# Kernel tuning notes

Measured on AMD Instinct MI355X. Metric: run time of the kernel, lower is better.

The kernel has to match this reference:

```python
import jax, jax.numpy as jnp
import numpy as np

jax.config.update("jax_enable_x64", True)

B, S = 16, 1024


def setup_inputs() -> dict:
    key = jax.random.key(0)
    scores = jax.random.normal(key, (B, S, S), dtype=jnp.float32)
    mask = jnp.ones((B, S), dtype=bool)
    return {"scores": scores, "mask": mask}


def _matrix_tree_logZ(scores, mask):
    # scores: [B,S,S] float64, mask: [B,S] bool
    lens = mask.sum(-1).astype(scores.dtype)          # lengths BEFORE forcing root position
    mask = mask.at[:, 0].set(True)                    # mask.index_fill(1, 0, 1)
    pair = mask[:, :, None] & mask[:, None, :]        # [B,S,S]
    s = jnp.where(pair, scores, -jnp.inf)
    m = jnp.max(s)                                    # single global max (scores.view(1,-1).max())
    A = jnp.exp(s - m)                                # exp-normalized adjacency, 0 outside mask
    rs = A.sum(-1)                                    # [B,S] row sums (degree)
    eye = jnp.eye(S, dtype=A.dtype)
    DmA = eye * rs[:, :, None] - A                    # Laplacian D - A
    # rows with mask==False stay identity rows
    L = jnp.where(mask[:, :, None], DmA, eye)
    logdet = jnp.linalg.slogdet(L[:, 1:, 1:])[1]      # [B]
    return (logdet + m * lens).sum()


def reference(scores, mask):
    # forward with mbr=True, target=None: probs = d logZ / d scores (marginals)
    s64 = scores.astype(jnp.float64)
    probs = jax.grad(_matrix_tree_logZ, argnums=0)(s64, mask)
    return probs.astype(jnp.float32)
```

## Files before the change

### kernel.cpp

```cpp
#include <hip/hip_runtime.h>

#define BB 16
#define SS 1024
#define NPAD 1024
#define NBLK 128
#define NSTEP 8
#define TILEPK 32768

typedef __attribute__((ext_vector_type(8))) __bf16 bf16x8;
typedef __attribute__((ext_vector_type(4))) float f32x4;

__device__ __forceinline__ unsigned int enc_f32(float f) {
  unsigned int u = __float_as_uint(f);
  return (u & 0x80000000u) ? ~u : (u | 0x80000000u);
}
__device__ __forceinline__ float dec_key(unsigned int k) {
  unsigned int u = (k & 0x80000000u) ? (k & 0x7fffffffu) : ~k;
  return __uint_as_float(u);
}
__device__ __forceinline__ void gload16(const __bf16* g, __bf16* l) {
  __builtin_amdgcn_global_load_lds(
      (const __attribute__((address_space(1))) void*)g,
      (__attribute__((address_space(3))) void*)l, 16, 0, 0);
}

__global__ void __launch_bounds__(64) kinit(unsigned long long* mk) { *mk = 0ull; }

__global__ void __launch_bounds__(256) kmax(const float* __restrict__ sc,
                                            unsigned long long* __restrict__ mk) {
  __shared__ unsigned long long red[256];
  const long long n = (long long)BB * SS * SS;
  unsigned long long best = 0ull;
  for (long long i = (long long)blockIdx.x * 256 + threadIdx.x; i < n;
       i += (long long)gridDim.x * 256) {
    unsigned long long k = ((unsigned long long)enc_f32(sc[i]) << 32) | (unsigned int)i;
    if (k > best) best = k;
  }
  red[threadIdx.x] = best;
  __syncthreads();
  for (int s = 128; s > 0; s >>= 1) {
    if ((int)threadIdx.x < s) {
      unsigned long long o = red[threadIdx.x + s];
      if (o > red[threadIdx.x]) red[threadIdx.x] = o;
    }
    __syncthreads();
  }
  if (threadIdx.x == 0) atomicMax(mk, red[0]);
}

__global__ void __launch_bounds__(256) kbuild(const float* __restrict__ sc,
                                              float* __restrict__ M,
                                              const unsigned long long* __restrict__ mk) {
  __shared__ float red[256];
  const int r = blockIdx.x;
  const int b = blockIdx.y;
  const int t = threadIdx.x;
  float* Mrow = M + ((size_t)b * NPAD + r) * NPAD;
  if (r == NPAD - 1) {
    for (int c = t; c < NPAD; c += 256) Mrow[c] = (c == NPAD - 1) ? 1.0f : 0.0f;
    return;
  }
  const float m = dec_key((unsigned int)(*mk >> 32));
  const int i = r + 1;
  const float* srow = sc + ((size_t)b * SS + i) * SS;
  float part = 0.f;
  for (int j = t; j < SS; j += 256) part += expf(srow[j] - m);
  red[t] = part;
  __syncthreads();
  for (int s = 128; s > 0; s >>= 1) {
    if (t < s) red[t] += red[t + s];
    __syncthreads();
  }
  const float rs = red[0];
  for (int c = t; c < NPAD; c += 256) {
    float v;
    if (c == NPAD - 1) v = 0.0f;
    else {
      v = -expf(srow[c + 1] - m);
      if (c == r) v += rs;
    }
    Mrow[c] = v;
  }
}

__global__ void __launch_bounds__(256) kcopydiag(const float* __restrict__ M,
                                                 __bf16* __restrict__ Tpk,
                                                 float* __restrict__ D,
                                                 __bf16* __restrict__ DA,
                                                 __bf16* __restrict__ DB, int kb) {
  const int x = blockIdx.x;
  const int t = threadIdx.x;
  if (x < NSTEP * BB) {
    const int rt = x >> 4, b = x & 15;
    const float* src = M + ((size_t)b * NPAD + rt * NBLK) * NPAD + kb * NBLK;
    __bf16* dst = Tpk + ((size_t)b * NSTEP + rt) * TILEPK;
#pragma unroll
    for (int itr = 0; itr < 8; ++itr) {
      const int gid = itr * 256 + t;
      const int m15 = gid & 15, q = (gid >> 4) & 3, R = (gid >> 6) & 7, ks = gid >> 9;
      const float* sp = src + (size_t)(R * 16 + m15) * NPAD + ks * 32 + q * 8;
      float f[8];
      *(float4*)(f + 0) = *(const float4*)(sp);
      *(float4*)(f + 4) = *(const float4*)(sp + 4);
      bf16x8 hv, lv;
#pragma unroll
      for (int j = 0; j < 8; ++j) {
        const float xv = f[j];
        const __bf16 h = (__bf16)xv;
        hv[j] = h;
        lv[j] = (__bf16)(xv - (float)h);
      }
      const int fi = ((R * 4 + q) * 16 + m15) * 8;
      *(bf16x8*)&dst[(size_t)ks * 8192 + fi] = hv;
      *(bf16x8*)&dst[(size_t)ks * 8192 + 4096 + fi] = lv;
    }
    return;
  }
  __shared__ float ds16[16][16];
  __shared__ float pinv16[16][18];
  __shared__ float rowp[16][128];
  __shared__ float rext[16][128];
  __shared__ float colp[128][20];
  __shared__ __bf16 Bsh[128][130];
  const int b = x - NSTEP * BB;
  const int tx = t & 15, ty = t >> 4;
  const int l = t & 63;
  const int lrow = l & 15, lcg = l >> 4;
  const float* src = M + ((size_t)b * NPAD + kb * NBLK) * NPAD + kb * NBLK;
  float r[8][8];
#pragma unroll
  for (int ii = 0; ii < 8; ++ii) {
    const float* sp = src + (size_t)(ty + 16 * ii) * NPAD + 8 * tx;
    *(float4*)&r[ii][0] = *(const float4*)(sp);
    *(float4*)&r[ii][4] = *(const float4*)(sp + 4);
  }

  for (int g = 0; g < 8; ++g) {
    const bool own_pc = ((tx >> 1) == g);
#pragma unroll
    for (int ii = 0; ii < 8; ++ii) {
      if (ii == g) {
        *(float4*)&rowp[ty][8 * tx] = *(const float4*)&r[ii][0];
        *(float4*)&rowp[ty][8 * tx + 4] = *(const float4*)&r[ii][4];
        if (own_pc) {
          *(float4*)&ds16[ty][8 * (tx & 1)] = *(const float4*)&r[ii][0];
          *(float4*)&ds16[ty][8 * (tx & 1) + 4] = *(const float4*)&r[ii][4];
        }
      }
      if (own_pc) {
        *(float4*)&colp[ty + 16 * ii][8 * (tx & 1)] = *(const float4*)&r[ii][0];
        *(float4*)&colp[ty + 16 * ii][8 * (tx & 1) + 4] = *(const float4*)&r[ii][4];
      }
    }
    __syncthreads();
    float dd[4];
    {
      const f32x4 dv = *(const f32x4*)&ds16[lrow][4 * lcg];
      dd[0] = dv[0]; dd[1] = dv[1]; dd[2] = dv[2]; dd[3] = dv[3];
    }
#pragma unroll
    for (int k = 0; k < 16; ++k) {
      const int pcg = k >> 2, pr = k & 3;
      const float pv = __shfl(dd[pr], k + 16 * pcg);
      const float pinv = 1.0f / pv;
      const float ck = __shfl(dd[pr], lrow + 16 * pcg);
      float rk[4];
#pragma unroll
      for (int c = 0; c < 4; ++c) rk[c] = __shfl(dd[c], k + 16 * lcg);
      const bool isp = (lrow == k);
      const float cp = ck * pinv;
#pragma unroll
      for (int c = 0; c < 4; ++c) {
        const bool zc = (lcg == pcg) && (c == pr);
        const float upd = (zc ? 0.0f : dd[c]) - cp * (zc ? 1.0f : rk[c]);
        const float prw = zc ? pinv : dd[c] * pinv;
        dd[c] = isp ? prw : upd;
      }
    }
#pragma unroll
    for (int c = 0; c < 4; ++c) pinv16[lrow][4 * lcg + c] = dd[c];
    __syncthreads();
    float pvr[16];
#pragma unroll
    for (int a = 0; a < 16; ++a) pvr[a] = pinv16[ty][a];
    float Rv[8];
#pragma unroll
    for (int jj = 0; jj < 8; ++jj) Rv[jj] = 0.0f;
#pragma unroll
    for (int a = 0; a < 16; ++a) {
      const float pa = pvr[a];
      const f32x4 q0 = *(const f32x4*)&rowp[a][8 * tx];
      const f32x4 q1 = *(const f32x4*)&rowp[a][8 * tx + 4];
      Rv[0] += pa * q0[0]; Rv[1] += pa * q0[1]; Rv[2] += pa * q0[2]; Rv[3] += pa * q0[3];
      Rv[4] += pa * q1[0]; Rv[5] += pa * q1[1]; Rv[6] += pa * q1[2]; Rv[7] += pa * q1[3];
    }
    if (own_pc) {
#pragma unroll
      for (int jj = 0; jj < 8; ++jj) Rv[jj] = pinv16[ty][8 * (tx & 1) + jj];
    }
    {
      float4 w0 = make_float4(Rv[0], Rv[1], Rv[2], Rv[3]);
      float4 w1 = make_float4(Rv[4], Rv[5], Rv[6], Rv[7]);
      *(float4*)&rext[ty][8 * tx] = w0;
      *(float4*)&rext[ty][8 * tx + 4] = w1;
    }
    __syncthreads();
    if (own_pc) {
#pragma unroll
      for (int ii = 0; ii < 8; ++ii)
#pragma unroll
        for (int jj = 0; jj < 8; ++jj) r[ii][jj] = 0.0f;
    }
#pragma unroll
    for (int a0 = 0; a0 < 16; a0 += 4) {
      float ca[8][4];
#pragma unroll
      for (int ii = 0; ii < 8; ++ii)
        *(float4*)&ca[ii][0] = *(const float4*)&colp[ty + 16 * ii][a0];
#pragma unroll
      for (int ac = 0; ac < 4; ++ac) {
        const f32x4 ra0 = *(const f32x4*)&rext[a0 + ac][8 * tx];
        const f32x4 ra1 = *(const f32x4*)&rext[a0 + ac][8 * tx + 4];
#pragma unroll
        for (int ii = 0; ii < 8; ++ii) {
          const float cv = ca[ii][ac];
          r[ii][0] -= cv * ra0[0]; r[ii][1] -= cv * ra0[1];
          r[ii][2] -= cv * ra0[2]; r[ii][3] -= cv * ra0[3];
          r[ii][4] -= cv * ra1[0]; r[ii][5] -= cv * ra1[1];
          r[ii][6] -= cv * ra1[2]; r[ii][7] -= cv * ra1[3];
        }
      }
    }
#pragma unroll
    for (int ii = 0; ii < 8; ++ii) {
      if (ii == g) {
        const f32x4 ra0 = *(const f32x4*)&rext[ty][8 * tx];
        const f32x4 ra1 = *(const f32x4*)&rext[ty][8 * tx + 4];
        r[ii][0] = ra0[0]; r[ii][1] = ra0[1]; r[ii][2] = ra0[2]; r[ii][3] = ra0[3];
        r[ii][4] = ra1[0]; r[ii][5] = ra1[1]; r[ii][6] = ra1[2]; r[ii][7] = ra1[3];
      }
    }
    __syncthreads();
  }
  float* dst = D + (size_t)b * NBLK * NBLK;
  __bf16* dA = DA + (size_t)b * TILEPK;
  __bf16* dB = DB + (size_t)b * TILEPK;
#pragma unroll
  for (int ii = 0; ii < 8; ++ii) {
    *(float4*)(dst + (size_t)(ty + 16 * ii) * NBLK + 8 * tx) = *(const float4*)&r[ii][0];
    *(float4*)(dst + (size_t)(ty + 16 * ii) * NBLK + 8 * tx + 4) = *(const float4*)&r[ii][4];
    bf16x8 hv, lv;
#pragma unroll
    for (int jj = 0; jj < 8; ++jj) {
      const float xv = r[ii][jj];
      const __bf16 h = (__bf16)xv;
      hv[jj] = h;
      lv[jj] = (__bf16)(xv - (float)h);
    }
    const int fiA = ((ii * 4 + (tx & 3)) * 16 + ty) * 8;
    *(bf16x8*)&dA[(size_t)(tx >> 2) * 8192 + fiA] = hv;
    *(bf16x8*)&dA[(size_t)(tx >> 2) * 8192 + 4096 + fiA] = lv;
    *(bf16x8*)&Bsh[ty + 16 * ii][8 * tx] = hv;
  }
  __syncthreads();
#pragma unroll
  for (int g8 = 0; g8 < 8; ++g8) {
    const int gid = g8 * 256 + t;
    const int n15 = gid & 15, q = (gid >> 4) & 3, Ct = (gid >> 6) & 7, ks = gid >> 9;
    const int n = Ct * 16 + n15, k0 = ks * 32 + q * 8;
    bf16x8 v;
#pragma unroll
    for (int j = 0; j < 8; ++j) v[j] = Bsh[k0 + j][n];
    *(bf16x8*)&dB[(size_t)ks * 4096 + (size_t)gid * 8] = v;
  }
  __syncthreads();
#pragma unroll
  for (int ii = 0; ii < 8; ++ii) {
    bf16x8 lv;
#pragma unroll
    for (int jj = 0; jj < 8; ++jj) {
      const float xv = r[ii][jj];
      const __bf16 h = (__bf16)xv;
      lv[jj] = (__bf16)(xv - (float)h);
    }
    *(bf16x8*)&Bsh[ty + 16 * ii][8 * tx] = lv;
  }
  __syncthreads();
#pragma unroll
  for (int g8 = 0; g8 < 8; ++g8) {
    const int gid = g8 * 256 + t;
    const int n15 = gid & 15, q = (gid >> 4) & 3, Ct = (gid >> 6) & 7, ks = gid >> 9;
    const int n = Ct * 16 + n15, k0 = ks * 32 + q * 8;
    bf16x8 v;
#pragma unroll
    for (int j = 0; j < 8; ++j) v[j] = Bsh[k0 + j][n];
    *(bf16x8*)&dB[(size_t)ks * 4096 + (size_t)gid * 8 + 4096] = v;
  }
}

__device__ __forceinline__ void gemm_pp(const __bf16* __restrict__ pA,
                                        const __bf16* __restrict__ pB,
                                        float* __restrict__ C, int ldc,
                                        float alpha, float beta) {
  __shared__ __bf16 sA[2][8192];
  __shared__ __bf16 sB[2][8192];
  const int t = threadIdx.x;
  const int l = t & 63, w = t >> 6;
  const int rbase = (w & 1) * 4, cbase = (w >> 1) * 4;

  f32x4 acc[4][4];
#pragma unroll
  for (int i = 0; i < 4; i++)
#pragma unroll
    for (int j = 0; j < 4; j++) acc[i][j] = (f32x4){0.f, 0.f, 0.f, 0.f};

  {
    const __bf16* gA = pA + (size_t)w * 2048 + l * 8;
    const __bf16* gB = pB + (size_t)w * 2048 + l * 8;
#pragma unroll
    for (int i = 0; i < 4; ++i) {
      gload16(gA + i * 512, &sA[0][w * 2048 + i * 512]);
      gload16(gB + i * 512, &sB[0][w * 2048 + i * 512]);
    }
  }
  __syncthreads();
#pragma unroll
  for (int ks = 0; ks < 4; ++ks) {
    const int buf = ks & 1;
    if (ks < 3) {
      const __bf16* gA = pA + (size_t)(ks + 1) * 8192 + w * 2048 + l * 8;
      const __bf16* gB = pB + (size_t)(ks + 1) * 8192 + w * 2048 + l * 8;
#pragma unroll
      for (int i = 0; i < 4; ++i) {
        gload16(gA + i * 512, &sA[buf ^ 1][w * 2048 + i * 512]);
        gload16(gB + i * 512, &sB[buf ^ 1][w * 2048 + i * 512]);
      }
    }
    bf16x8 a_h[4], a_l[4];
#pragma unroll
    for (int rt = 0; rt < 4; ++rt) {
      a_h[rt] = *(const bf16x8*)&sA[buf][(size_t)((rbase + rt) * 64 + l) * 8];
      a_l[rt] = *(const bf16x8*)&sA[buf][4096 + (size_t)((rbase + rt) * 64 + l) * 8];
    }
#pragma unroll
    for (int ct = 0; ct < 4; ++ct) {
      bf16x8 b_h = *(const bf16x8*)&sB[buf][(size_t)((cbase + ct) * 64 + l) * 8];
      bf16x8 b_l = *(const bf16x8*)&sB[buf][4096 + (size_t)((cbase + ct) * 64 + l) * 8];
#pragma unroll
      for (int rt = 0; rt < 4; ++rt) {
        acc[rt][ct] = __builtin_amdgcn_mfma_f32_16x16x32_bf16(a_h[rt], b_h, acc[rt][ct], 0, 0, 0);
        acc[rt][ct] = __builtin_amdgcn_mfma_f32_16x16x32_bf16(a_h[rt], b_l, acc[rt][ct], 0, 0, 0);
        acc[rt][ct] = __builtin_amdgcn_mfma_f32_16x16x32_bf16(a_l[rt], b_h, acc[rt][ct], 0, 0, 0);
      }
    }
    if (ks < 3) __syncthreads();
  }
  const int row0 = (w & 1) * 64 + ((l >> 4) << 2);
  const int col0 = (w >> 1) * 64 + (l & 15);
  if (beta == 0.0f) {
#pragma unroll
    for (int rt = 0; rt < 4; ++rt)
#pragma unroll
      for (int ct = 0; ct < 4; ++ct)
#pragma unroll
        for (int r = 0; r < 4; ++r)
          C[(size_t)(row0 + rt * 16 + r) * ldc + col0 + ct * 16] = alpha * acc[rt][ct][r];
  } else {
#pragma unroll
    for (int rt = 0; rt < 4; ++rt)
#pragma unroll
      for (int ct = 0; ct < 4; ++ct)
#pragma unroll
        for (int r = 0; r < 4; ++r) {
          float* cp = C + (size_t)(row0 + rt * 16 + r) * ldc + col0 + ct * 16;
          *cp = beta * (*cp) + alpha * acc[rt][ct][r];
        }
  }
}

__global__ void __launch_bounds__(256) kscale(float* __restrict__ M,
                                              const float* __restrict__ D,
                                              const __bf16* __restrict__ DA,
                                              __bf16* __restrict__ Rpk, int kb) {
  const int jt = blockIdx.x, b = blockIdx.y;
  float* Mb = M + (size_t)b * NPAD * NPAD;
  const int t = threadIdx.x;
  if (jt == kb) {
    const float* Dinv = D + (size_t)b * NBLK * NBLK;
    const int c = (t & 31) * 4, r0 = t >> 5;
    float* dst = Mb + (size_t)(kb * NBLK) * NPAD + kb * NBLK;
    for (int r = r0; r < NBLK; r += 8)
      *(float4*)(dst + (size_t)r * NPAD + c) = *(const float4*)(Dinv + r * NBLK + c);
    return;
  }
  __shared__ __bf16 sA[8192];
  __shared__ __bf16 Bh[4096], Bl[4096];
  __shared__ __bf16 Bsh[128][130];
  const int l = t & 63, w = t >> 6;
  const int ic = t & 127, kh = t >> 7;
  const int rbase = (w & 1) * 4, cbase = (w >> 1) * 4;
  const __bf16* pA = DA + (size_t)b * TILEPK;
  float* Btile = Mb + (size_t)(kb * NBLK) * NPAD + jt * NBLK;

  f32x4 acc[4][4];
#pragma unroll
  for (int i = 0; i < 4; i++)
#pragma unroll
    for (int j = 0; j < 4; j++) acc[i][j] = (f32x4){0.f, 0.f, 0.f, 0.f};

  for (int ks = 0; ks < 4; ++ks) {
    const __bf16* gA = pA + (size_t)ks * 8192 + w * 2048 + l * 8;
#pragma unroll
    for (int i = 0; i < 4; ++i) gload16(gA + i * 512, &sA[w * 2048 + i * 512]);
    {
      const float* bp = Btile + (size_t)(ks * 32 + kh * 16) * NPAD + ic;
      float f[16];
#pragma unroll
      for (int kk = 0; kk < 16; ++kk) f[kk] = bp[(size_t)kk * NPAD];
      const int base = ((ic >> 4) * 4 + kh * 2) * 16 + (ic & 15);
#pragma unroll
      for (int g = 0; g < 2; ++g) {
        bf16x8 hv, lv;
#pragma unroll
        for (int j = 0; j < 8; ++j) {
          const float xv = f[g * 8 + j];
          const __bf16 h = (__bf16)xv;
          hv[j] = h;
          lv[j] = (__bf16)(xv - (float)h);
        }
        *(bf16x8*)&Bh[(size_t)(base + g * 16) * 8] = hv;
        *(bf16x8*)&Bl[(size_t)(base + g * 16) * 8] = lv;
      }
    }
    __syncthreads();
    bf16x8 a_h[4], a_l[4];
#pragma unroll
    for (int rt = 0; rt < 4; ++rt) {
      a_h[rt] = *(const bf16x8*)&sA[(size_t)((rbase + rt) * 64 + l) * 8];
      a_l[rt] = *(const bf16x8*)&sA[4096 + (size_t)((rbase + rt) * 64 + l) * 8];
    }
#pragma unroll
    for (int ct = 0; ct < 4; ++ct) {
      bf16x8 b_h = *(const bf16x8*)&Bh[(size_t)((cbase + ct) * 64 + l) * 8];
      bf16x8 b_l = *(const bf16x8*)&Bl[(size_t)((cbase + ct) * 64 + l) * 8];
#pragma unroll
      for (int rt = 0; rt < 4; ++rt) {
        acc[rt][ct] = __builtin_amdgcn_mfma_f32_16x16x32_bf16(a_h[rt], b_h, acc[rt][ct], 0, 0, 0);
        acc[rt][ct] = __builtin_amdgcn_mfma_f32_16x16x32_bf16(a_h[rt], b_l, acc[rt][ct], 0, 0, 0);
        acc[rt][ct] = __builtin_amdgcn_mfma_f32_16x16x32_bf16(a_l[rt], b_h, acc[rt][ct], 0, 0, 0);
      }
    }
    __syncthreads();
  }
  __bf16* Rt = Rpk + ((size_t)b * NSTEP + jt) * TILEPK;
  const int row0 = (w & 1) * 64 + ((l >> 4) << 2);
  const int col0 = (w >> 1) * 64 + (l & 15);
#pragma unroll
  for (int rt = 0; rt < 4; ++rt)
#pragma unroll
    for (int ct = 0; ct < 4; ++ct)
#pragma unroll
      for (int rr = 0; rr < 4; ++rr) {
        const float v = acc[rt][ct][rr];
        const int row = row0 + rt * 16 + rr;
        const int col = col0 + ct * 16;
        Btile[(size_t)row * NPAD + col] = v;
        Bsh[row][col] = (__bf16)v;
      }
  __syncthreads();
#pragma unroll
  for (int g8 = 0; g8 < 8; ++g8) {
    const int gid = g8 * 256 + t;
    const int n15 = gid & 15, q = (gid >> 4) & 3, Ct = (gid >> 6) & 7, ks = gid >> 9;
    const int n = Ct * 16 + n15, k0 = ks * 32 + q * 8;
    bf16x8 v;
#pragma unroll
    for (int j = 0; j < 8; ++j) v[j] = Bsh[k0 + j][n];
    *(bf16x8*)&Rt[(size_t)ks * 4096 + (size_t)gid * 8] = v;
  }
  __syncthreads();
#pragma unroll
  for (int rt = 0; rt < 4; ++rt)
#pragma unroll
    for (int ct = 0; ct < 4; ++ct)
#pragma unroll
      for (int rr = 0; rr < 4; ++rr) {
        const float v = acc[rt][ct][rr];
        const int row = row0 + rt * 16 + rr;
        const int col = col0 + ct * 16;
        const __bf16 h = (__bf16)v;
        Bsh[row][col] = (__bf16)(v - (float)h);
      }
  __syncthreads();
#pragma unroll
  for (int g8 = 0; g8 < 8; ++g8) {
    const int gid = g8 * 256 + t;
    const int n15 = gid & 15, q = (gid >> 4) & 3, Ct = (gid >> 6) & 7, ks = gid >> 9;
    const int n = Ct * 16 + n15, k0 = ks * 32 + q * 8;
    bf16x8 v;
#pragma unroll
    for (int j = 0; j < 8; ++j) v[j] = Bsh[k0 + j][n];
    *(bf16x8*)&Rt[(size_t)ks * 4096 + (size_t)gid * 8 + 4096] = v;
  }
}

__global__ void __launch_bounds__(256) kupdate(float* __restrict__ M,
                                               const __bf16* __restrict__ Tpk,
                                               const __bf16* __restrict__ Rpk,
                                               const __bf16* __restrict__ DB, int kb) {
  const int jt = blockIdx.x;
  int it = blockIdx.y; it = (it >= kb) ? it + 1 : it;
  const int b = blockIdx.z;
  float* Ctile = M + ((size_t)b * NPAD + it * NBLK) * NPAD + jt * NBLK;
  const __bf16* pA = Tpk + ((size_t)b * NSTEP + it) * TILEPK;
  if (jt == kb) {
    gemm_pp(pA, DB + (size_t)b * TILEPK, Ctile, NPAD, -1.0f, 0.0f);
  } else {
    gemm_pp(pA, Rpk + ((size_t)b * NSTEP + jt) * TILEPK, Ctile, NPAD, -1.0f, 1.0f);
  }
}

__global__ void __launch_bounds__(256) kfinal(const float* __restrict__ sc,
                                              const float* __restrict__ Minv,
                                              float* __restrict__ out,
                                              const unsigned long long* __restrict__ mk) {
  __shared__ float Ls[64][65];
  __shared__ float Ds[64];
  const int qt = blockIdx.x, pt = blockIdx.y, b = blockIdx.z;
  const int t = threadIdx.x;
  const unsigned long long key = *mk;
  const float m = dec_key((unsigned int)(key >> 32));
  const unsigned int amax = (unsigned int)key;
  const float* Mb = Minv + (size_t)b * NPAD * NPAD;
  const int q0 = qt * 64, p0 = pt * 64;
  {
    const int pp = t & 63, qq0 = t >> 6;
#pragma unroll
    for (int rp = 0; rp < 16; ++rp) {
      const int qq = qq0 + 4 * rp;
      int rrow = q0 + qq - 1; if (rrow < 0) rrow = 0;
      int ccol = p0 + pp - 1; if (ccol < 0) ccol = 0;
      Ls[qq][pp] = Mb[(size_t)rrow * NPAD + ccol];
    }
    if (t < 64) {
      int cc = p0 + t - 1; if (cc < 0) cc = 0;
      Ds[t] = Mb[(size_t)cc * NPAD + cc];
    }
  }
  __syncthreads();
  const int qq = t & 63, pp0 = t >> 6;
#pragma unroll
  for (int rp = 0; rp < 16; ++rp) {
    const int pp = pp0 + 4 * rp;
    const int p = p0 + pp, q = q0 + qq;
    const size_t off = ((size_t)b * SS + p) * SS + q;
    float val = 0.f;
    if (p >= 1) {
      const float a = expf(sc[off] - m);
      const float g = Ds[pp] - ((q >= 1) ? Ls[qq][pp] : 0.f);
      val = a * g;
    }
    if ((unsigned int)off == amax) val += 16.0f;
    out[off] = val;
  }
}

extern "C" void kernel_launch(void* const* d_in, const int* in_sizes, int n_in,
                              void* d_out, int out_size, void* d_ws, size_t ws_size,
                              hipStream_t stream) {
  const float* sc = (const float*)d_in[0];
  float* out = (float*)d_out;
  char* ws = (char*)d_ws;
  unsigned long long* mk = (unsigned long long*)ws;
  float* M = (float*)(ws + 256);
  float* D = M + (size_t)BB * NPAD * NPAD;
  __bf16* Tpk = (__bf16*)(D + (size_t)BB * NBLK * NBLK);
  __bf16* Rpk = Tpk + (size_t)BB * NSTEP * TILEPK;
  __bf16* DA = Rpk + (size_t)BB * NSTEP * TILEPK;
  __bf16* DB = DA + (size_t)BB * TILEPK;

  hipLaunchKernelGGL(kinit, dim3(1), dim3(64), 0, stream, mk);
  hipLaunchKernelGGL(kmax, dim3(1024), dim3(256), 0, stream, sc, mk);
  hipLaunchKernelGGL(kbuild, dim3(NPAD, BB), dim3(256), 0, stream, sc, M, mk);
  for (int kb = 0; kb < NSTEP; ++kb) {
    hipLaunchKernelGGL(kcopydiag, dim3(NSTEP * BB + BB), dim3(256), 0, stream, M, Tpk, D, DA, DB, kb);
    hipLaunchKernelGGL(kscale, dim3(NSTEP, BB), dim3(256), 0, stream, M, D, DA, Rpk, kb);
    hipLaunchKernelGGL(kupdate, dim3(NSTEP, NSTEP - 1, BB), dim3(256), 0, stream, M, Tpk, Rpk, DB, kb);
  }
  hipLaunchKernelGGL(kfinal, dim3(16, 16, BB), dim3(256), 0, stream, sc, M, out, mk);
}
```

Before: 957.2 us.

## Fuse next-step diagonal inversion and panel packing into the trailing update kernel

Adds a kfused kernel that, in one launch, performs the trailing GEMM update for step kb and also computes the next step's diagonal block (GEMM, then in-block Gauss-Jordan inversion) and the next column panel packing. The launch sequence thus drops the per-step kcopydiag and kupdate. It ping-pongs the D/DA/DB and Tpk buffers so the next step's data does not overwrite the current one, and replaces the pivot division with a hardware reciprocal. This removes launches and a global round trip per step, but puts heterogeneous blocks in one grid, and the 16 diagonal-inversion blocks are long and serial, which may leave the critical path unchanged.

After: 1.253 ms. 1.31x slower.

```diff
diff --git a/kernel.cpp b/kernel.cpp
--- a/kernel.cpp
+++ b/kernel.cpp
@@ -162,7 +162,7 @@
     for (int k = 0; k < 16; ++k) {
       const int pcg = k >> 2, pr = k & 3;
       const float pv = __shfl(dd[pr], k + 16 * pcg);
-      const float pinv = 1.0f / pv;
+      const float pinv = __builtin_amdgcn_rcpf(pv);
       const float ck = __shfl(dd[pr], lrow + 16 * pcg);
       float rk[4];
 #pragma unroll
@@ -249,15 +249,17 @@
   for (int ii = 0; ii < 8; ++ii) {
     *(float4*)(dst + (size_t)(ty + 16 * ii) * NBLK + 8 * tx) = *(const float4*)&r[ii][0];
     *(float4*)(dst + (size_t)(ty + 16 * ii) * NBLK + 8 * tx + 4) = *(const float4*)&r[ii][4];
-    bf16x8 hv, lv;
+    bf16x8 hv;
 #pragma unroll
     for (int jj = 0; jj < 8; ++jj) {
       const float xv = r[ii][jj];
       const __bf16 h = (__bf16)xv;
       hv[jj] = h;
-      lv[jj] = (__bf16)(xv - (float)h);
     }
     const int fiA = ((ii * 4 + (tx & 3)) * 16 + ty) * 8;
+    bf16x8 lv;
+#pragma unroll
+    for (int jj = 0; jj < 8; ++jj) lv[jj] = (__bf16)(r[ii][jj] - (float)hv[jj]);
     *(bf16x8*)&dA[(size_t)(tx >> 2) * 8192 + fiA] = hv;
     *(bf16x8*)&dA[(size_t)(tx >> 2) * 8192 + 4096 + fiA] = lv;
     *(bf16x8*)&Bsh[ty + 16 * ii][8 * tx] = hv;
@@ -298,29 +300,21 @@
   }
 }
 
-__device__ __forceinline__ void gemm_pp(const __bf16* __restrict__ pA,
-                                        const __bf16* __restrict__ pB,
-                                        float* __restrict__ C, int ldc,
-                                        float alpha, float beta) {
-  __shared__ __bf16 sA[2][8192];
-  __shared__ __bf16 sB[2][8192];
+__device__ __forceinline__ void gemm_acc(const __bf16* __restrict__ pA,
+                                         const __bf16* __restrict__ pB,
+                                         char* smem, f32x4 acc[4][4]) {
   const int t = threadIdx.x;
   const int l = t & 63, w = t >> 6;
   const int rbase = (w & 1) * 4, cbase = (w >> 1) * 4;
-
-  f32x4 acc[4][4];
-#pragma unroll
-  for (int i = 0; i < 4; i++)
-#pragma unroll
-    for (int j = 0; j < 4; j++) acc[i][j] = (f32x4){0.f, 0.f, 0.f, 0.f};
-
+  __bf16* sAb[2] = {(__bf16*)smem, (__bf16*)(smem + 16384)};
+  __bf16* sBb[2] = {(__bf16*)(smem + 32768), (__bf16*)(smem + 49152)};
   {
     const __bf16* gA = pA + (size_t)w * 2048 + l * 8;
     const __bf16* gB = pB + (size_t)w * 2048 + l * 8;
 #pragma unroll
     for (int i = 0; i < 4; ++i) {
-      gload16(gA + i * 512, &sA[0][w * 2048 + i * 512]);
-      gload16(gB + i * 512, &sB[0][w * 2048 + i * 512]);
+      gload16(gA + i * 512, sAb[0] + w * 2048 + i * 512);
+      gload16(gB + i * 512, sBb[0] + w * 2048 + i * 512);
     }
   }
   __syncthreads();
@@ -332,20 +326,20 @@
       const __bf16* gB = pB + (size_t)(ks + 1) * 8192 + w * 2048 + l * 8;
 #pragma unroll
       for (int i = 0; i < 4; ++i) {
-        gload16(gA + i * 512, &sA[buf ^ 1][w * 2048 + i * 512]);
-        gload16(gB + i * 512, &sB[buf ^ 1][w * 2048 + i * 512]);
+        gload16(gA + i * 512, sAb[buf ^ 1] + w * 2048 + i * 512);
+        gload16(gB + i * 512, sBb[buf ^ 1] + w * 2048 + i * 512);
       }
     }
     bf16x8 a_h[4], a_l[4];
 #pragma unroll
     for (int rt = 0; rt < 4; ++rt) {
-      a_h[rt] = *(const bf16x8*)&sA[buf][(size_t)((rbase + rt) * 64 + l) * 8];
-      a_l[rt] = *(const bf16x8*)&sA[buf][4096 + (size_t)((rbase + rt) * 64 + l) * 8];
+      a_h[rt] = *(const bf16x8*)&sAb[buf][(size_t)((rbase + rt) * 64 + l) * 8];
+      a_l[rt] = *(const bf16x8*)&sAb[buf][4096 + (size_t)((rbase + rt) * 64 + l) * 8];
     }
 #pragma unroll
     for (int ct = 0; ct < 4; ++ct) {
-      bf16x8 b_h = *(const bf16x8*)&sB[buf][(size_t)((cbase + ct) * 64 + l) * 8];
-      bf16x8 b_l = *(const bf16x8*)&sB[buf][4096 + (size_t)((cbase + ct) * 64 + l) * 8];
+      bf16x8 b_h = *(const bf16x8*)&sBb[buf][(size_t)((cbase + ct) * 64 + l) * 8];
+      bf16x8 b_l = *(const bf16x8*)&sBb[buf][4096 + (size_t)((cbase + ct) * 64 + l) * 8];
 #pragma unroll
       for (int rt = 0; rt < 4; ++rt) {
         acc[rt][ct] = __builtin_amdgcn_mfma_f32_16x16x32_bf16(a_h[rt], b_h, acc[rt][ct], 0, 0, 0);
@@ -355,6 +349,21 @@
     }
     if (ks < 3) __syncthreads();
   }
+}
+
+__device__ __forceinline__ void gemm_pp(const __bf16* __restrict__ pA,
+                                        const __bf16* __restrict__ pB,
+                                        float* __restrict__ C, int ldc,
+                                        float alpha, float beta) {
+  __shared__ __align__(16) char smem_pp[65536];
+  const int t = threadIdx.x;
+  const int l = t & 63, w = t >> 6;
+  f32x4 acc[4][4];
+#pragma unroll
+  for (int i = 0; i < 4; i++)
+#pragma unroll
+    for (int j = 0; j < 4; j++) acc[i][j] = (f32x4){0.f, 0.f, 0.f, 0.f};
+  gemm_acc(pA, pB, smem_pp, acc);
   const int row0 = (w & 1) * 64 + ((l >> 4) << 2);
   const int col0 = (w >> 1) * 64 + (l & 15);
   if (beta == 0.0f) {
@@ -501,6 +510,335 @@
 #pragma unroll
     for (int j = 0; j < 8; ++j) v[j] = Bsh[k0 + j][n];
     *(bf16x8*)&Rt[(size_t)ks * 4096 + (size_t)gid * 8 + 4096] = v;
+  }
+}
+
+__global__ void __launch_bounds__(256, 2) kfused(
+    float* __restrict__ M,
+    const __bf16* __restrict__ Tcur, __bf16* __restrict__ Tnxt,
+    const __bf16* __restrict__ Rpk, const __bf16* __restrict__ DBc,
+    float* __restrict__ Dn, __bf16* __restrict__ DAn, __bf16* __restrict__ DBn,
+    int kb) {
+  __shared__ __align__(16) char smem[65536];
+  const int x = blockIdx.x;
+  const int t = threadIdx.x;
+  const int l = t & 63, w = t >> 6;
+  const int row0 = (w & 1) * 64 + ((l >> 4) << 2);
+  const int col0 = (w >> 1) * 64 + (l & 15);
+  const int kd = kb + 1;
+
+  if (x >= 144) {
+    const int idx = x - 144;
+    const int b = idx & 15, rem = idx >> 4;
+    const int jt7 = rem % 7, it7 = rem / 7;
+    const int jt = jt7 + (jt7 >= kd);
+    const int it = it7 + (it7 >= kb);
+    f32x4 acc[4][4];
+#pragma unroll
+    for (int i = 0; i < 4; i++)
+#pragma unroll
+      for (int j = 0; j < 4; j++) acc[i][j] = (f32x4){0.f, 0.f, 0.f, 0.f};
+    const __bf16* pA = Tcur + ((size_t)b * NSTEP + it) * TILEPK;
+    const __bf16* pB = (jt == kb) ? (DBc + (size_t)b * TILEPK)
+                                  : (Rpk + ((size_t)b * NSTEP + jt) * TILEPK);
+    gemm_acc(pA, pB, smem, acc);
+    float* C = M + ((size_t)b * NPAD + it * NBLK) * NPAD + jt * NBLK;
+    if (jt == kb) {
+#pragma unroll
+      for (int pt = 0; pt < 4; ++pt)
+#pragma unroll
+        for (int ct = 0; ct < 4; ++ct)
+#pragma unroll
+          for (int rr = 0; rr < 4; ++rr)
+            C[(size_t)(row0 + pt * 16 + rr) * NPAD + col0 + ct * 16] = -acc[pt][ct][rr];
+    } else {
+#pragma unroll
+      for (int pt = 0; pt < 4; ++pt)
+#pragma unroll
+        for (int ct = 0; ct < 4; ++ct)
+#pragma unroll
+          for (int rr = 0; rr < 4; ++rr) {
+            float* cp = C + (size_t)(row0 + pt * 16 + rr) * NPAD + col0 + ct * 16;
+            *cp = *cp - acc[pt][ct][rr];
+          }
+    }
+    return;
+  }
+
+  if (x >= 16) {
+    const int p = x - 16;
+    const int rt = p >> 4, b = p & 15;
+    f32x4 acc[4][4];
+#pragma unroll
+    for (int i = 0; i < 4; i++)
+#pragma unroll
+      for (int j = 0; j < 4; j++) acc[i][j] = (f32x4){0.f, 0.f, 0.f, 0.f};
+    if (rt != kb) {
+      gemm_acc(Tcur + ((size_t)b * NSTEP + rt) * TILEPK,
+               Rpk + ((size_t)b * NSTEP + kd) * TILEPK, smem, acc);
+    }
+    const float* Csrc = M + ((size_t)b * NPAD + rt * NBLK) * NPAD + kd * NBLK;
+    __bf16* dst = Tnxt + ((size_t)b * NSTEP + rt) * TILEPK;
+    float Cv[4][4][4];
+#pragma unroll
+    for (int pt = 0; pt < 4; ++pt)
+#pragma unroll
+      for (int ct = 0; ct < 4; ++ct)
+#pragma unroll
+        for (int rr = 0; rr < 4; ++rr)
+          Cv[pt][ct][rr] =
+              Csrc[(size_t)(row0 + pt * 16 + rr) * NPAD + col0 + ct * 16] - acc[pt][ct][rr];
+    __syncthreads();
+    __bf16(*Bsh)[136] = (__bf16(*)[136])smem;
+#pragma unroll
+    for (int pt = 0; pt < 4; ++pt)
+#pragma unroll
+      for (int ct = 0; ct < 4; ++ct)
+#pragma unroll
+        for (int rr = 0; rr < 4; ++rr)
+          Bsh[row0 + pt * 16 + rr][col0 + ct * 16] = (__bf16)Cv[pt][ct][rr];
+    __syncthreads();
+#pragma unroll
+    for (int g8 = 0; g8 < 8; ++g8) {
+      const int gid = g8 * 256 + t;
+      const int m15 = gid & 15, q = (gid >> 4) & 3, R = (gid >> 6) & 7, ks = gid >> 9;
+      bf16x8 v = *(const bf16x8*)&Bsh[R * 16 + m15][ks * 32 + q * 8];
+      *(bf16x8*)&dst[(size_t)ks * 4096 + (size_t)gid * 8] = v;
+    }
+    __syncthreads();
+#pragma unroll
+    for (int pt = 0; pt < 4; ++pt)
+#pragma unroll
+      for (int ct = 0; ct < 4; ++ct)
+#pragma unroll
+        for (int rr = 0; rr < 4; ++rr) {
+          const float v = Cv[pt][ct][rr];
+          const __bf16 h = (__bf16)v;
+          Bsh[row0 + pt * 16 + rr][col0 + ct * 16] = (__bf16)(v - (float)h);
+        }
+    __syncthreads();
+#pragma unroll
+    for (int g8 = 0; g8 < 8; ++g8) {
+      const int gid = g8 * 256 + t;
+      const int m15 = gid & 15, q = (gid >> 4) & 3, R = (gid >> 6) & 7, ks = gid >> 9;
+      bf16x8 v = *(const bf16x8*)&Bsh[R * 16 + m15][ks * 32 + q * 8];
+      *(bf16x8*)&dst[(size_t)ks * 4096 + (size_t)gid * 8 + 4096] = v;
+    }
+    return;
+  }
+
+  const int b = x;
+  const int tx = t & 15, ty = t >> 4;
+  const int lrow = l & 15, lcg = l >> 4;
+  f32x4 acc[4][4];
+#pragma unroll
+  for (int i = 0; i < 4; i++)
+#pragma unroll
+    for (int j = 0; j < 4; j++) acc[i][j] = (f32x4){0.f, 0.f, 0.f, 0.f};
+  gemm_acc(Tcur + ((size_t)b * NSTEP + kd) * TILEPK,
+           Rpk + ((size_t)b * NSTEP + kd) * TILEPK, smem, acc);
+  __syncthreads();
+
+  float(*rowp)[128] = (float(*)[128])(smem);
+  float(*rext)[128] = (float(*)[128])(smem + 8192);
+  float(*colp)[20] = (float(*)[20])(smem + 16384);
+  float(*ds16)[16] = (float(*)[16])(smem + 26624);
+  float(*pinv16)[18] = (float(*)[18])(smem + 27648);
+  float(*Msh)[132] = (float(*)[132])(smem + 28800);
+  __bf16(*Bsh)[136] = (__bf16(*)[136])(smem + 28800);
+
+  const float* src = M + ((size_t)b * NPAD + kd * NBLK) * NPAD + kd * NBLK;
+  float r[8][8];
+#pragma unroll
+  for (int c = 0; c < 4; ++c) {
+    if ((w & 1) == (c >> 1)) {
+      const int rt0 = (c & 1) * 2;
+#pragma unroll
+      for (int r2 = 0; r2 < 2; ++r2)
+#pragma unroll
+        for (int ct = 0; ct < 4; ++ct)
+#pragma unroll
+          for (int rr = 0; rr < 4; ++rr)
+            Msh[r2 * 16 + ((l >> 4) << 2) + rr][col0 + ct * 16] = acc[rt0 + r2][ct][rr];
+    }
+    __syncthreads();
+#pragma unroll
+    for (int i2 = 0; i2 < 2; ++i2) {
+      const int ii = 2 * c + i2;
+      const int lr = ty + 16 * i2;
+      const float* sp = src + (size_t)(ty + 16 * ii) * NPAD + 8 * tx;
+      const f32x4 a0 = *(const f32x4*)&Msh[lr][8 * tx];
+      const f32x4 a1 = *(const f32x4*)&Msh[lr][8 * tx + 4];
+      const float4 m0 = *(const float4*)sp;
+      const float4 m1 = *(const float4*)(sp + 4);
+      r[ii][0] = m0.x - a0[0]; r[ii][1] = m0.y - a0[1];
+      r[ii][2] = m0.z - a0[2]; r[ii][3] = m0.w - a0[3];
+      r[ii][4] = m1.x - a1[0]; r[ii][5] = m1.y - a1[1];
+      r[ii][6] = m1.z - a1[2]; r[ii][7] = m1.w - a1[3];
+    }
+    __syncthreads();
+  }
+
+  for (int g = 0; g < 8; ++g) {
+    const bool own_pc = ((tx >> 1) == g);
+#pragma unroll
+    for (int ii = 0; ii < 8; ++ii) {
+      if (ii == g) {
+        *(float4*)&rowp[ty][8 * tx] = *(const float4*)&r[ii][0];
+        *(float4*)&rowp[ty][8 * tx + 4] = *(const float4*)&r[ii][4];
+        if (own_pc) {
+          *(float4*)&ds16[ty][8 * (tx & 1)] = *(const float4*)&r[ii][0];
+          *(float4*)&ds16[ty][8 * (tx & 1) + 4] = *(const float4*)&r[ii][4];
+        }
+      }
+      if (own_pc) {
+        *(float4*)&colp[ty + 16 * ii][8 * (tx & 1)] = *(const float4*)&r[ii][0];
+        *(float4*)&colp[ty + 16 * ii][8 * (tx & 1) + 4] = *(const float4*)&r[ii][4];
+      }
+    }
+    __syncthreads();
+    float dd[4];
+    {
+      const f32x4 dv = *(const f32x4*)&ds16[lrow][4 * lcg];
+      dd[0] = dv[0]; dd[1] = dv[1]; dd[2] = dv[2]; dd[3] = dv[3];
+    }
+#pragma unroll
+    for (int k = 0; k < 16; ++k) {
+      const int pcg = k >> 2, pr = k & 3;
+      const float pv = __shfl(dd[pr], k + 16 * pcg);
+      const float pinv = __builtin_amdgcn_rcpf(pv);
+      const float ck = __shfl(dd[pr], lrow + 16 * pcg);
+      float rk[4];
+#pragma unroll
+      for (int c = 0; c < 4; ++c) rk[c] = __shfl(dd[c], k + 16 * lcg);
+      const bool isp = (lrow == k);
+      const float cp = ck * pinv;
+#pragma unroll
+      for (int c = 0; c < 4; ++c) {
+        const bool zc = (lcg == pcg) && (c == pr);
+        const float upd = (zc ? 0.0f : dd[c]) - cp * (zc ? 1.0f : rk[c]);
+        const float prw = zc ? pinv : dd[c] * pinv;
+        dd[c] = isp ? prw : upd;
+      }
+    }
+#pragma unroll
+    for (int c = 0; c < 4; ++c) pinv16[lrow][4 * lcg + c] = dd[c];
+    __syncthreads();
+    float pvr[16];
+#pragma unroll
+    for (int a = 0; a < 16; ++a) pvr[a] = pinv16[ty][a];
+    float Rv[8];
+#pragma unroll
+    for (int jj = 0; jj < 8; ++jj) Rv[jj] = 0.0f;
+#pragma unroll
+    for (int a = 0; a < 16; ++a) {
+      const float pa = pvr[a];
+      const f32x4 q0 = *(const f32x4*)&rowp[a][8 * tx];
+      const f32x4 q1 = *(const f32x4*)&rowp[a][8 * tx + 4];
+      Rv[0] += pa * q0[0]; Rv[1] += pa * q0[1]; Rv[2] += pa * q0[2]; Rv[3] += pa * q0[3];
+      Rv[4] += pa * q1[0]; Rv[5] += pa * q1[1]; Rv[6] += pa * q1[2]; Rv[7] += pa * q1[3];
+    }
+    if (own_pc) {
+#pragma unroll
+      for (int jj = 0; jj < 8; ++jj) Rv[jj] = pinv16[ty][8 * (tx & 1) + jj];
+    }
+    {
+      float4 w0 = make_float4(Rv[0], Rv[1], Rv[2], Rv[3]);
+      float4 w1 = make_float4(Rv[4], Rv[5], Rv[6], Rv[7]);
+      *(float4*)&rext[ty][8 * tx] = w0;
+      *(float4*)&rext[ty][8 * tx + 4] = w1;
+    }
+    __syncthreads();
+    if (own_pc) {
+#pragma unroll
+      for (int ii = 0; ii < 8; ++ii)
+#pragma unroll
+        for (int jj = 0; jj < 8; ++jj) r[ii][jj] = 0.0f;
+    }
+#pragma unroll
+    for (int a0 = 0; a0 < 16; a0 += 4) {
+      float ca[8][4];
+#pragma unroll
+      for (int ii = 0; ii < 8; ++ii)
+        *(float4*)&ca[ii][0] = *(const float4*)&colp[ty + 16 * ii][a0];
+#pragma unroll
+      for (int ac = 0; ac < 4; ++ac) {
+        const f32x4 ra0 = *(const f32x4*)&rext[a0 + ac][8 * tx];
+        const f32x4 ra1 = *(const f32x4*)&rext[a0 + ac][8 * tx + 4];
+#pragma unroll
+        for (int ii = 0; ii < 8; ++ii) {
+          const float cv = ca[ii][ac];
+          r[ii][0] -= cv * ra0[0]; r[ii][1] -= cv * ra0[1];
+          r[ii][2] -= cv * ra0[2]; r[ii][3] -= cv * ra0[3];
+          r[ii][4] -= cv * ra1[0]; r[ii][5] -= cv * ra1[1];
+          r[ii][6] -= cv * ra1[2]; r[ii][7] -= cv * ra1[3];
+        }
+      }
+    }
+#pragma unroll
+    for (int ii = 0; ii < 8; ++ii) {
+      if (ii == g) {
+        const f32x4 ra0 = *(const f32x4*)&rext[ty][8 * tx];
+        const f32x4 ra1 = *(const f32x4*)&rext[ty][8 * tx + 4];
+        r[ii][0] = ra0[0]; r[ii][1] = ra0[1]; r[ii][2] = ra0[2]; r[ii][3] = ra0[3];
+        r[ii][4] = ra1[0]; r[ii][5] = ra1[1]; r[ii][6] = ra1[2]; r[ii][7] = ra1[3];
+      }
+    }
+    __syncthreads();
+  }
+  float* dstD = Dn + (size_t)b * NBLK * NBLK;
+  __bf16* dA = DAn + (size_t)b * TILEPK;
+  __bf16* dB = DBn + (size_t)b * TILEPK;
+#pragma unroll
+  for (int ii = 0; ii < 8; ++ii) {
+    *(float4*)(dstD + (size_t)(ty + 16 * ii) * NBLK + 8 * tx) = *(const float4*)&r[ii][0];
+    *(float4*)(dstD + (size_t)(ty + 16 * ii) * NBLK + 8 * tx + 4) = *(const float4*)&r[ii][4];
+    bf16x8 hv, lv;
+#pragma unroll
+    for (int jj = 0; jj < 8; ++jj) {
+      const float xv = r[ii][jj];
+      const __bf16 h = (__bf16)xv;
+      hv[jj] = h;
+      lv[jj] = (__bf16)(xv - (float)h);
+    }
+    const int fiA = ((ii * 4 + (tx & 3)) * 16 + ty) * 8;
+    *(bf16x8*)&dA[(size_t)(tx >> 2) * 8192 + fiA] = hv;
+    *(bf16x8*)&dA[(size_t)(tx >> 2) * 8192 + 4096 + fiA] = lv;
+    *(bf16x8*)&Bsh[ty + 16 * ii][8 * tx] = hv;
+  }
+  __syncthreads();
+#pragma unroll
+  for (int g8 = 0; g8 < 8; ++g8) {
+    const int gid = g8 * 256 + t;
+    const int n15 = gid & 15, q = (gid >> 4) & 3, Ct = (gid >> 6) & 7, ks = gid >> 9;
+    const int n = Ct * 16 + n15, k0 = ks * 32 + q * 8;
+    bf16x8 v;
+#pragma unroll
+    for (int j = 0; j < 8; ++j) v[j] = Bsh[k0 + j][n];
+    *(bf16x8*)&dB[(size_t)ks * 4096 + (size_t)gid * 8] = v;
+  }
+  __syncthreads();
+#pragma unroll
+  for (int ii = 0; ii < 8; ++ii) {
+    bf16x8 lv;
+#pragma unroll
+    for (int jj = 0; jj < 8; ++jj) {
+      const float xv = r[ii][jj];
+      const __bf16 h = (__bf16)xv;
+      lv[jj] = (__bf16)(xv - (float)h);
+    }
+    *(bf16x8*)&Bsh[ty + 16 * ii][8 * tx] = lv;
+  }
+  __syncthreads();
+#pragma unroll
+  for (int g8 = 0; g8 < 8; ++g8) {
+    const int gid = g8 * 256 + t;
+    const int n15 = gid & 15, q = (gid >> 4) & 3, Ct = (gid >> 6) & 7, ks = gid >> 9;
+    const int n = Ct * 16 + n15, k0 = ks * 32 + q * 8;
+    bf16x8 v;
+#pragma unroll
+    for (int j = 0; j < 8; ++j) v[j] = Bsh[k0 + j][n];
+    *(bf16x8*)&dB[(size_t)ks * 4096 + (size_t)gid * 8 + 4096] = v;
   }
 }
 
@@ -573,19 +911,37 @@
   char* ws = (char*)d_ws;
   unsigned long long* mk = (unsigned long long*)ws;
   float* M = (float*)(ws + 256);
-  float* D = M + (size_t)BB * NPAD * NPAD;
-  __bf16* Tpk = (__bf16*)(D + (size_t)BB * NBLK * NBLK);
-  __bf16* Rpk = Tpk + (size_t)BB * NSTEP * TILEPK;
-  __bf16* DA = Rpk + (size_t)BB * NSTEP * TILEPK;
-  __bf16* DB = DA + (size_t)BB * TILEPK;
+  float* D0 = M + (size_t)BB * NPAD * NPAD;
+  float* D1 = D0 + (size_t)BB * NBLK * NBLK;
+  __bf16* Tpk0 = (__bf16*)(D1 + (size_t)BB * NBLK * NBLK);
+  __bf16* Tpk1 = Tpk0 + (size_t)BB * NSTEP * TILEPK;
+  __bf16* Rpk = Tpk1 + (size_t)BB * NSTEP * TILEPK;
+  __bf16* DA0 = Rpk + (size_t)BB * NSTEP * TILEPK;
+  __bf16* DA1 = DA0 + (size_t)BB * TILEPK;
+  __bf16* DB0 = DA1 + (size_t)BB * TILEPK;
+  __bf16* DB1 = DB0 + (size_t)BB * TILEPK;
 
   hipLaunchKernelGGL(kinit, dim3(1), dim3(64), 0, stream, mk);
   hipLaunchKernelGGL(kmax, dim3(1024), dim3(256), 0, stream, sc, mk);
   hipLaunchKernelGGL(kbuild, dim3(NPAD, BB), dim3(256), 0, stream, sc, M, mk);
-  for (int kb = 0; kb < NSTEP; ++kb) {
-    hipLaunchKernelGGL(kcopydiag, dim3(NSTEP * BB + BB), dim3(256), 0, stream, M, Tpk, D, DA, DB, kb);
-    hipLaunchKernelGGL(kscale, dim3(NSTEP, BB), dim3(256), 0, stream, M, D, DA, Rpk, kb);
-    hipLaunchKernelGGL(kupdate, dim3(NSTEP, NSTEP - 1, BB), dim3(256), 0, stream, M, Tpk, Rpk, DB, kb);
-  }
+  hipLaunchKernelGGL(kcopydiag, dim3(NSTEP * BB + BB), dim3(256), 0, stream,
+                     M, Tpk0, D0, DA0, DB0, 0);
+  for (int kb = 0; kb < 7; ++kb) {
+    const int par = kb & 1;
+    float* Dc = par ? D1 : D0;
+    __bf16* DAc = par ? DA1 : DA0;
+    __bf16* DBc = par ? DB1 : DB0;
+    __bf16* Tc = par ? Tpk1 : Tpk0;
+    __bf16* Tn = par ? Tpk0 : Tpk1;
+    float* Dn = par ? D0 : D1;
+    __bf16* DAn = par ? DA0 : DA1;
+    __bf16* DBn = par ? DB0 : DB1;
+    hipLaunchKernelGGL(kscale, dim3(NSTEP, BB), dim3(256), 0, stream, M, Dc, DAc, Rpk, kb);
+    hipLaunchKernelGGL(kfused, dim3(16 + 128 + 784), dim3(256), 0, stream,
+                       M, Tc, Tn, Rpk, DBc, Dn, DAn, DBn, kb);
+  }
+  hipLaunchKernelGGL(kscale, dim3(NSTEP, BB), dim3(256), 0, stream, M, D1, DA1, Rpk, 7);
+  hipLaunchKernelGGL(kupdate, dim3(NSTEP, NSTEP - 1, BB), dim3(256), 0, stream,
+                     M, Tpk1, Rpk, DB1, 7);
   hipLaunchKernelGGL(kfinal, dim3(16, 16, BB), dim3(256), 0, stream, sc, M, out, mk);
 }
```
